# Optimization experiments

Hardware: AMD Instinct MI355X
Metric: run time of the kernel (lower is better)

Reference implementation:

```python
import jax, jax.numpy as jnp
import numpy as np

N = 200000      # number of source simplices (columns of B)
M_SEG = 100000  # number of target simplices (rows of B)
NNZ = 400000    # ~2 nonzeros per column for a boundary operator
C_IN = 256
C_OUT = 256


def setup_inputs() -> dict:
    key = jax.random.key(0)
    k1, k2, k3, k4, k5 = jax.random.split(key, 5)
    x_src = jax.random.normal(k1, (N, C_IN), dtype=jnp.float32)
    W = jax.random.normal(k2, (C_IN, C_OUT), dtype=jnp.float32) / np.sqrt(C_IN)
    b_vals = jax.random.normal(k3, (NNZ,), dtype=jnp.float32)
    b_rows = jax.random.randint(k4, (NNZ,), 0, M_SEG, dtype=jnp.int32)
    b_cols = jax.random.randint(k5, (NNZ,), 0, N, dtype=jnp.int32)
    return {"x_src": x_src, "W": W, "b_vals": b_vals,
            "b_rows": b_rows, "b_cols": b_cols, "M": M_SEG}


def reference(x_src, W, b_vals, b_rows, b_cols, M):
    # Dense projection: nn.Linear(in, out, bias=False) -> x @ W
    x_proj = x_src @ W                                  # [N, C_out]
    # Sparse boundary matmul: out[r] += v * x_proj[c] for each (r, c, v) in B
    msgs = b_vals[:, None] * x_proj[b_cols]             # [nnz, C_out] gather
    out = jax.ops.segment_sum(msgs, b_rows, num_segments=M)  # [M, C_out] scatter-add
    return out
```

## Files before the change

### kernel.cpp

```cpp
#include <hip/hip_runtime.h>


typedef short bf16x8 __attribute__((ext_vector_type(8)));
typedef float f32x4  __attribute__((ext_vector_type(4)));

static __device__ __forceinline__ unsigned short f2bf(float f) {
    union { float f; unsigned u; } a; a.f = f;
    unsigned r = a.u + 0x7FFFu + ((a.u >> 16) & 1u);
    return (unsigned short)(r >> 16);
}

static __device__ __forceinline__ float bf2f(unsigned short h) {
    union { unsigned u; float f; } a; a.u = (unsigned)h << 16;
    return a.f;
}

static __device__ __forceinline__ unsigned pack2(float f0, float f1) {
    return (unsigned)f2bf(f0) | ((unsigned)f2bf(f1) << 16);
}

static __device__ __forceinline__ bf16x8 cvt8(float4 lo, float4 hi) {
    union { bf16x8 v; unsigned u[4]; } r;
    r.u[0] = pack2(lo.x, lo.y);
    r.u[1] = pack2(lo.z, lo.w);
    r.u[2] = pack2(hi.x, hi.y);
    r.u[3] = pack2(hi.z, hi.w);
    return r.v;
}

__global__ __launch_bounds__(256) void wtrans_kernel(
    const float* __restrict__ W, unsigned short* __restrict__ Wt)
{
    int k = blockIdx.x;
    int n = threadIdx.x;
    Wt[(size_t)n * 256 + k] = f2bf(W[(size_t)k * 256 + n]);
}

__global__ __launch_bounds__(256) void hist_kernel(
    const int* __restrict__ b_rows, int* __restrict__ cnt, int nnz)
{
    int i = blockIdx.x * 256 + threadIdx.x;
    if (i < nnz) atomicAdd(&cnt[b_rows[i]], 1);
}

__global__ __launch_bounds__(1024) void scan_part_kernel(
    const int* __restrict__ cnt, int* __restrict__ partials, int M)
{
    int tid = threadIdx.x;
    int base = blockIdx.x * 4096;
    int s = 0;
    #pragma unroll
    for (int k = 0; k < 4; ++k) {
        int i = base + k * 1024 + tid;
        if (i < M) s += cnt[i];
    }
    #pragma unroll
    for (int d = 1; d < 64; d <<= 1) s += __shfl_xor(s, d);
    __shared__ int wsum[16];
    int lane = tid & 63, wid = tid >> 6;
    if (lane == 0) wsum[wid] = s;
    __syncthreads();
    if (tid == 0) {
        int t = 0;
        #pragma unroll
        for (int w = 0; w < 16; ++w) t += wsum[w];
        partials[blockIdx.x] = t;
    }
}

__global__ __launch_bounds__(64) void scan_mid_kernel(
    int* __restrict__ partials, int* __restrict__ off, int np, int M)
{
    int lane = threadIdx.x;
    int v = (lane < np) ? partials[lane] : 0;
    int x = v;
    #pragma unroll
    for (int d = 1; d < 64; d <<= 1) { int y = __shfl_up(x, d); if (lane >= d) x += y; }
    if (lane < np) partials[lane] = x - v;
    if (lane == 63) off[M] = x;
}

__global__ __launch_bounds__(1024) void scan_apply_kernel(
    const int* __restrict__ cnt, const int* __restrict__ partials,
    int* __restrict__ off, int* __restrict__ cursor, int M)
{
    int tid = threadIdx.x;
    int base = blockIdx.x * 4096 + tid * 4;
    int4 v = make_int4(0, 0, 0, 0);
    if (base + 3 < M) v = *reinterpret_cast<const int4*>(cnt + base);
    else {
        if (base + 0 < M) v.x = cnt[base + 0];
        if (base + 1 < M) v.y = cnt[base + 1];
        if (base + 2 < M) v.z = cnt[base + 2];
    }
    int s1 = v.x + v.y, s2 = s1 + v.z, tsum = s2 + v.w;
    int x = tsum;
    int lane = tid & 63, wid = tid >> 6;
    #pragma unroll
    for (int d = 1; d < 64; d <<= 1) { int y = __shfl_up(x, d); if (lane >= d) x += y; }
    __shared__ int wsum[16];
    if (lane == 63) wsum[wid] = x;
    __syncthreads();
    if (wid == 0 && lane < 16) {
        int w = wsum[lane];
        int xx = w;
        #pragma unroll
        for (int d = 1; d < 16; d <<= 1) { int y = __shfl_up(xx, d); if (lane >= d) xx += y; }
        wsum[lane] = xx - w;
    }
    __syncthreads();
    int excl = (x - tsum) + wsum[wid] + partials[blockIdx.x];
    int o0 = excl, o1 = excl + v.x, o2 = excl + s1, o3 = excl + s2;
    if (base + 0 < M) { off[base + 0] = o0; cursor[base + 0] = o0; }
    if (base + 1 < M) { off[base + 1] = o1; cursor[base + 1] = o1; }
    if (base + 2 < M) { off[base + 2] = o2; cursor[base + 2] = o2; }
    if (base + 3 < M) { off[base + 3] = o3; cursor[base + 3] = o3; }
}

__global__ __launch_bounds__(256) void fill_kernel(
    const float* __restrict__ b_vals, const int* __restrict__ b_rows,
    const int* __restrict__ b_cols, int* __restrict__ cursor,
    int* __restrict__ csr_col, float* __restrict__ csr_val, int nnz)
{
    int i = blockIdx.x * 256 + threadIdx.x;
    if (i < nnz) {
        int r = b_rows[i];
        int pos = atomicAdd(&cursor[r], 1);
        csr_col[pos] = b_cols[i];
        csr_val[pos] = b_vals[i];
    }
}

__global__ __launch_bounds__(512, 2) void proj2_kernel(
    const float* __restrict__ X, const unsigned short* __restrict__ Wt,
    unsigned short* __restrict__ xp, int ntiles, int tpw)
{
    __shared__ __align__(16) unsigned char wlds[256 * 512];

    int tid = threadIdx.x;
    int lane = tid & 63, wid = tid >> 6;

    const char* wtg = reinterpret_cast<const char*>(Wt);
    #pragma unroll
    for (int itc = 0; itc < 16; ++itc) {
        int c = tid + itc * 512;
        int n = c >> 5, j = c & 31;
        uint4 w16 = *reinterpret_cast<const uint4*>(wtg + (size_t)n * 512 + j * 16);
        int b = n * 512 + ((j * 16) ^ ((n & 7) << 4));
        *reinterpret_cast<uint4*>(wlds + b) = w16;
    }
    __syncthreads();

    int arow = lane & 15;
    int kg = lane >> 4;
    int xo = (arow & 7) << 4;

    for (int it = 0; it < tpw; ++it) {
        int tile = blockIdx.x * (tpw << 3) + (it << 3) + wid;
        if (tile >= ntiles) break;
        int R = tile * 16;

        const float* ap = X + (size_t)(R + arow) * 256 + kg * 8;
        float4 buf[16];
        #pragma unroll
        for (int s = 0; s < 8; ++s) {
            buf[2 * s]     = *reinterpret_cast<const float4*>(ap + s * 32);
            buf[2 * s + 1] = *reinterpret_cast<const float4*>(ap + s * 32 + 4);
        }

        f32x4 acc[16] = {};
        #pragma unroll
        for (int s = 0; s < 8; ++s) {
            bf16x8 a = cvt8(buf[2 * s], buf[2 * s + 1]);
            int koff = (s * 64 + kg * 16) ^ xo;
            #pragma unroll
            for (int nt = 0; nt < 16; ++nt) {
                int n = nt * 16 + arow;
                bf16x8 b = *reinterpret_cast<const bf16x8*>(wlds + n * 512 + koff);
                acc[nt] = __builtin_amdgcn_mfma_f32_16x16x32_bf16(a, b, acc[nt], 0, 0, 0);
            }
        }

        #pragma unroll
        for (int rr = 0; rr < 4; ++rr) {
            int row = R + kg * 4 + rr;
            #pragma unroll
            for (int g = 0; g < 4; ++g) {
                ushort4 h;
                h.x = f2bf(acc[4 * g + 0][rr]);
                h.y = f2bf(acc[4 * g + 1][rr]);
                h.z = f2bf(acc[4 * g + 2][rr]);
                h.w = f2bf(acc[4 * g + 3][rr]);
                *reinterpret_cast<ushort4*>(xp + (size_t)row * 256 + g * 64 + arow * 4) = h;
            }
        }
    }
}

__global__ __launch_bounds__(256) void gather_kernel(
    const unsigned short* __restrict__ xp, const float* __restrict__ csr_val,
    const int* __restrict__ csr_col, const int* __restrict__ off,
    float* __restrict__ out, int M)
{
    int row = blockIdx.x * 4 + (threadIdx.x >> 6);
    if (row >= M) return;
    int lane = threadIdx.x & 63;

    int s = off[row], e = off[row + 1];
    float a0 = 0.f, a1 = 0.f, a2 = 0.f, a3 = 0.f;

    for (int j = s; j < e; j += 8) {
        int nb = e - j;
        int c[8]; float v[8]; ushort4 xs[8];
        #pragma unroll
        for (int t = 0; t < 8; ++t)
            if (t < nb) { c[t] = csr_col[j + t]; v[t] = csr_val[j + t]; }
        #pragma unroll
        for (int t = 0; t < 8; ++t)
            if (t < nb)
                xs[t] = *reinterpret_cast<const ushort4*>(
                    xp + (size_t)c[t] * 256 + lane * 4);
        #pragma unroll
        for (int t = 0; t < 8; ++t)
            if (t < nb) {
                a0 += v[t] * bf2f(xs[t].x);
                a1 += v[t] * bf2f(xs[t].y);
                a2 += v[t] * bf2f(xs[t].z);
                a3 += v[t] * bf2f(xs[t].w);
            }
    }

    int col0 = (lane >> 4) * 64 + (lane & 15);
    float* o = out + (size_t)row * 256;
    o[col0 +  0] = a0;
    o[col0 + 16] = a1;
    o[col0 + 32] = a2;
    o[col0 + 48] = a3;
}

extern "C" void kernel_launch(void* const* d_in, const int* in_sizes, int n_in,
                              void* d_out, int out_size, void* d_ws, size_t ws_size,
                              hipStream_t stream) {
    const float* x_src  = (const float*)d_in[0];
    const float* W      = (const float*)d_in[1];
    const float* b_vals = (const float*)d_in[2];
    const int*   b_rows = (const int*)d_in[3];
    const int*   b_cols = (const int*)d_in[4];

    const int C = 256;
    const int M = out_size / C;
    const int nnz = in_sizes[2];
    const int N = in_sizes[0] / C;

    char* ws = (char*)d_ws;
    unsigned short* Wt = (unsigned short*)ws;           ws += 256 * 256 * 2;
    int*   cnt     = (int*)ws;                          ws += (size_t)M * 4;
    int*   off     = (int*)ws;                          ws += (size_t)(M + 1) * 4;
    int*   cursor  = (int*)ws;                          ws += (size_t)M * 4;
    int*   partials= (int*)ws;                          ws += 64 * 4;
    int*   csr_col = (int*)ws;                          ws += (size_t)nnz * 4;
    float* csr_val = (float*)ws;                        ws += (size_t)nnz * 4;
    ws = (char*)(((size_t)ws + 63) & ~(size_t)63);
    unsigned short* xp = (unsigned short*)ws;

    float* out = (float*)d_out;

    hipMemsetAsync(cnt, 0, (size_t)M * 4, stream);

    wtrans_kernel<<<256, 256, 0, stream>>>(W, Wt);

    int nblk_nnz = (nnz + 255) / 256;
    hist_kernel<<<nblk_nnz, 256, 0, stream>>>(b_rows, cnt, nnz);

    int nb = (M + 4095) / 4096;
    scan_part_kernel<<<nb, 1024, 0, stream>>>(cnt, partials, M);
    scan_mid_kernel<<<1, 64, 0, stream>>>(partials, off, nb, M);
    scan_apply_kernel<<<nb, 1024, 0, stream>>>(cnt, partials, off, cursor, M);

    fill_kernel<<<nblk_nnz, 256, 0, stream>>>(b_vals, b_rows, b_cols, cursor,
                                              csr_col, csr_val, nnz);

    int ntiles = N / 16;
    int grid_p = 256;
    int tpw = (ntiles + grid_p * 8 - 1) / (grid_p * 8);
    proj2_kernel<<<grid_p, 512, 0, stream>>>(x_src, Wt, xp, ntiles, tpw);

    gather_kernel<<<(M + 3) / 4, 256, 0, stream>>>(xp, csr_val, csr_col, off, out, M);
}
```

Baseline: 208.5 us.

## Restructure projection GEMM with register-resident W and async double-buffered X loads

Rewrites the dense projection kernel so each wave keeps its 64-column slice of W in registers instead of staging all of W in LDS. Tiles of X are streamed into a double-buffered LDS area with async global-to-LDS loads, so the next tile's fetch overlaps the current tile's MFMA work. Four waves now share one 16-row tile, each computing a quarter of the output columns. The cost is higher VGPR pressure from holding 32 bf16x8 B fragments per lane and a block-wide barrier every round.

```diff
diff --git a/kernel.cpp b/kernel.cpp
--- a/kernel.cpp
+++ b/kernel.cpp
@@ -3,6 +3,8 @@
 
 typedef short bf16x8 __attribute__((ext_vector_type(8)));
 typedef float f32x4  __attribute__((ext_vector_type(4)));
+
+#define PGRID 256
 
 static __device__ __forceinline__ unsigned short f2bf(float f) {
     union { float f; unsigned u; } a; a.f = f;
@@ -26,6 +28,13 @@
     r.u[2] = pack2(hi.x, hi.y);
     r.u[3] = pack2(hi.z, hi.w);
     return r.v;
+}
+
+static __device__ __forceinline__ void gload_lds16(const void* g, void* l) {
+    __builtin_amdgcn_global_load_lds(
+        (const __attribute__((address_space(1))) unsigned int*)g,
+        (__attribute__((address_space(3))) unsigned int*)l,
+        16, 0, 0);
 }
 
 __global__ __launch_bounds__(256) void wtrans_kernel(
@@ -131,69 +140,97 @@
     }
 }
 
-__global__ __launch_bounds__(512, 2) void proj2_kernel(
+__global__ __launch_bounds__(512, 2) void proj3_kernel(
     const float* __restrict__ X, const unsigned short* __restrict__ Wt,
-    unsigned short* __restrict__ xp, int ntiles, int tpw)
-{
-    __shared__ __align__(16) unsigned char wlds[256 * 512];
+    unsigned short* __restrict__ xp, int ntiles)
+{
+    __shared__ __align__(16) unsigned char abuf[2][2][16 * 1024];
 
     int tid = threadIdx.x;
-    int lane = tid & 63, wid = tid >> 6;
-
-    const char* wtg = reinterpret_cast<const char*>(Wt);
-    #pragma unroll
-    for (int itc = 0; itc < 16; ++itc) {
-        int c = tid + itc * 512;
-        int n = c >> 5, j = c & 31;
-        uint4 w16 = *reinterpret_cast<const uint4*>(wtg + (size_t)n * 512 + j * 16);
-        int b = n * 512 + ((j * 16) ^ ((n & 7) << 4));
-        *reinterpret_cast<uint4*>(wlds + b) = w16;
-    }
-    __syncthreads();
-
+    int lane = tid & 63, w = tid >> 6;
+    int grp = w >> 2;
+    int ww  = w & 3;
     int arow = lane & 15;
     int kg = lane >> 4;
-    int xo = (arow & 7) << 4;
-
-    for (int it = 0; it < tpw; ++it) {
-        int tile = blockIdx.x * (tpw << 3) + (it << 3) + wid;
-        if (tile >= ntiles) break;
-        int R = tile * 16;
-
-        const float* ap = X + (size_t)(R + arow) * 256 + kg * 8;
-        float4 buf[16];
-        #pragma unroll
-        for (int s = 0; s < 8; ++s) {
-            buf[2 * s]     = *reinterpret_cast<const float4*>(ap + s * 32);
-            buf[2 * s + 1] = *reinterpret_cast<const float4*>(ap + s * 32 + 4);
+
+    bf16x8 b[4][8];
+    {
+        const char* wt = reinterpret_cast<const char*>(Wt);
+        size_t nb = (size_t)(ww * 64 + arow) * 512 + kg * 16;
+        #pragma unroll
+        for (int nt = 0; nt < 4; ++nt)
+            #pragma unroll
+            for (int s = 0; s < 8; ++s)
+                b[nt][s] = *reinterpret_cast<const bf16x8*>(
+                    wt + nb + (size_t)nt * 16 * 512 + s * 64);
+    }
+
+    const char* Xb = reinterpret_cast<const char*>(X);
+    int gid = blockIdx.x * 2 + grp;
+    const int stride = PGRID * 2;
+    int rounds = (ntiles + stride - 1) / stride;
+
+    int swz = (lane * 16);
+
+    {
+        int tile = gid;
+        if (tile < ntiles) {
+            #pragma unroll
+            for (int ii = 0; ii < 4; ++ii) {
+                int i = ww * 4 + ii;
+                const void* src = Xb + (size_t)(tile * 16 + i) * 1024
+                                     + (swz ^ ((i & 7) << 4));
+                gload_lds16(src, &abuf[0][grp][i * 1024]);
+            }
         }
-
-        f32x4 acc[16] = {};
-        #pragma unroll
-        for (int s = 0; s < 8; ++s) {
-            bf16x8 a = cvt8(buf[2 * s], buf[2 * s + 1]);
-            int koff = (s * 64 + kg * 16) ^ xo;
+    }
+    __syncthreads();
+
+    for (int r = 0; r < rounds; ++r) {
+        int tile = gid + r * stride;
+        int p = r & 1;
+
+        {
+            int ntile = gid + (r + 1) * stride;
+            if (ntile < ntiles) {
+                #pragma unroll
+                for (int ii = 0; ii < 4; ++ii) {
+                    int i = ww * 4 + ii;
+                    const void* src = Xb + (size_t)(ntile * 16 + i) * 1024
+                                         + (swz ^ ((i & 7) << 4));
+                    gload_lds16(src, &abuf[p ^ 1][grp][i * 1024]);
+                }
+            }
+        }
+
+        if (tile < ntiles) {
+            const unsigned char* ab = abuf[p][grp];
+            int rx = arow * 1024;
+            int xo = (arow & 7) << 4;
+            f32x4 acc[4] = {};
             #pragma unroll
-            for (int nt = 0; nt < 16; ++nt) {
-                int n = nt * 16 + arow;
-                bf16x8 b = *reinterpret_cast<const bf16x8*>(wlds + n * 512 + koff);
-                acc[nt] = __builtin_amdgcn_mfma_f32_16x16x32_bf16(a, b, acc[nt], 0, 0, 0);
+            for (int s = 0; s < 8; ++s) {
+                int base = kg * 32 + s * 128;
+                float4 lo = *reinterpret_cast<const float4*>(ab + rx + ((base +  0) ^ xo));
+                float4 hi = *reinterpret_cast<const float4*>(ab + rx + ((base + 16) ^ xo));
+                bf16x8 a = cvt8(lo, hi);
+                #pragma unroll
+                for (int nt = 0; nt < 4; ++nt)
+                    acc[nt] = __builtin_amdgcn_mfma_f32_16x16x32_bf16(a, b[nt][s], acc[nt], 0, 0, 0);
+            }
+            int R = tile * 16;
+            #pragma unroll
+            for (int rr = 0; rr < 4; ++rr) {
+                int row = R + kg * 4 + rr;
+                ushort4 h;
+                h.x = f2bf(acc[0][rr]);
+                h.y = f2bf(acc[1][rr]);
+                h.z = f2bf(acc[2][rr]);
+                h.w = f2bf(acc[3][rr]);
+                *reinterpret_cast<ushort4*>(xp + (size_t)row * 256 + ww * 64 + arow * 4) = h;
             }
         }
-
-        #pragma unroll
-        for (int rr = 0; rr < 4; ++rr) {
-            int row = R + kg * 4 + rr;
-            #pragma unroll
-            for (int g = 0; g < 4; ++g) {
-                ushort4 h;
-                h.x = f2bf(acc[4 * g + 0][rr]);
-                h.y = f2bf(acc[4 * g + 1][rr]);
-                h.z = f2bf(acc[4 * g + 2][rr]);
-                h.w = f2bf(acc[4 * g + 3][rr]);
-                *reinterpret_cast<ushort4*>(xp + (size_t)row * 256 + g * 64 + arow * 4) = h;
-            }
-        }
+        __syncthreads();
     }
 }
 
@@ -281,9 +318,7 @@
                                               csr_col, csr_val, nnz);
 
     int ntiles = N / 16;
-    int grid_p = 256;
-    int tpw = (ntiles + grid_p * 8 - 1) / (grid_p * 8);
-    proj2_kernel<<<grid_p, 512, 0, stream>>>(x_src, Wt, xp, ntiles, tpw);
+    proj3_kernel<<<PGRID, 512, 0, stream>>>(x_src, Wt, xp, ntiles);
 
     gather_kernel<<<(M + 3) / 4, 256, 0, stream>>>(xp, csr_val, csr_col, off, out, M);
 }
```

Measured after the change: 198.5 us. 1.05x faster.
